# Kernel optimization log

Measured on AMD Instinct MI355X. Metric: run time of the kernel, lower is better.

The kernel has to match this reference:

```python
import jax, jax.numpy as jnp
import numpy as np

H, W = 800, 800          # map height/width (Encoder init args)
B, N, SD = 1, 100000, 32 # batch, entity_num, scatter_dim
C = 8                    # number of spatial grids
SPATIAL = (120, 120)     # SPATIAL_SIZE


def setup_inputs() -> dict:
    key = jax.random.key(0)
    ks = jax.random.split(key, 8)
    return {
        "spatial": jax.random.normal(ks[0], (C, H, W), jnp.float32) * 200.0,
        "project_embeddings": jax.random.normal(ks[1], (B, N, SD), jnp.float32),
        "locations": jax.random.randint(ks[2], (B, N, 2), 0, 800, jnp.int64 if jax.config.jax_enable_x64 else jnp.int32),
        "scalar": jax.random.normal(ks[3], (B, 8), jnp.float32),
        "w1": jax.random.normal(ks[4], (8, 32), jnp.float32) * 0.35,
        "b1": jnp.zeros((32,), jnp.float32),
        "w2": jax.random.normal(ks[5], (32, 4), jnp.float32) * 0.25,
        "b2": jnp.zeros((4,), jnp.float32),
    }


def _scatter_connection(project_embeddings, locations):
    # project_embeddings: [B, N, SD], locations: [B, N, 2] (x, y) ints
    loc = locations.reshape(-1, 2)
    x = jnp.clip(loc[:, 0], 0, W - 1)
    y = jnp.clip(loc[:, 1], 0, H - 1)
    bias = jnp.repeat(jnp.arange(B, dtype=x.dtype), N) * (H * W)
    idx = y * W + x + bias                       # [B*N] flat indices into B*H*W
    src = project_embeddings.reshape(-1, SD).T   # [SD, B*N]
    smap = jnp.zeros((SD, B * H * W), project_embeddings.dtype)
    smap = smap.at[:, idx].add(src)              # duplicate-safe scatter_add
    smap = smap.reshape(SD, B, H, W).transpose(1, 0, 2, 3)  # [B, SD, H, W]
    return jax.image.resize(smap, (B, SD) + SPATIAL, method="bilinear")


def _process_grids(spatial):
    # crop is the full map (grid of ones -> all rows/cols kept)
    arr = jnp.nan_to_num(spatial, posinf=0.0)
    arr = jnp.where(arr > 255.0, 255.0, arr) / 255.0
    arr = jnp.rot90(arr, k=1, axes=(1, 2))       # torch rot90 default: CCW in last-2 dims
    arr = jax.image.resize(arr, (C,) + SPATIAL, method="bilinear")
    return arr.astype(jnp.float32)[None]         # [1, C, 120, 120]


def reference(spatial, project_embeddings, locations, scalar, w1, b1, w2, b2):
    scatter_entity = _scatter_connection(project_embeddings, locations)  # [B,32,120,120]
    processed_spatial = _process_grids(spatial)                          # [1, C,120,120]
    final_spatial = jnp.concatenate([processed_spatial, scatter_entity], axis=1)
    scalar_embeddings = jax.nn.relu(scalar @ w1 + b1)
    scalar_embeddings = jax.nn.relu(scalar_embeddings @ w2 + b2)
    return final_spatial, scalar_embeddings
```

## Files before the change

### kernel.cpp

```cpp
#include <hip/hip_runtime.h>
#include <hip/hip_bf16.h>
#include <math.h>

#define HMAP 800
#define WMAP 800
#define OHW  120
#define NCELL (OHW * OHW)
#define NCH  8
#define NPTS 100000
#define SDIM 32
#define CAP  16
#define NBIN1 121
#define NBINS (NBIN1 * NBIN1)

__device__ __forceinline__ float rscale() { return 800.0f / 120.0f; }

__device__ __forceinline__ float clipval(float v) {
    if (isnan(v)) v = 0.f;
    else if (isinf(v)) v = (v > 0.f) ? 0.f : -3.4028234663852886e38f;
    if (v > 255.f) v = 255.f;
    return v;
}

__device__ __forceinline__ float norm_sum(int i) {
    const float r = rscale();
    float c = ((float)i + 0.5f) * r - 0.5f;
    int j0 = (int)ceilf(c - r);
    float s = 0.f;
#pragma unroll
    for (int k = 0; k < 14; ++k) {
        int j = j0 + k;
        if (j < 0 || j >= HMAP) continue;
        s += fmaxf(0.f, 1.f - fabsf(c - (float)j) / r);
    }
    return s;
}

#define WS_COUNTS   0
#define WS_SPILLCUR 14641
#define WS_INVS     14656
#define WS_ENTRIES  14784
#define WS_SPILL    (WS_ENTRIES + NBINS * CAP * 2)
#define WS_T        (WS_SPILL + NPTS * 2)
#define WS_END      (WS_T + NCH * WMAP * OHW)
#define WS_REQ_BYTES ((size_t)WS_END * 4)

#define Z_BLOCKS    58
#define FILLB       ((NPTS + 1023) / 1024)
#define RY_BLOCKS   (NCH * WMAP / 2)
#define GA_BLOCKS   (NCELL / 4)
#define RX_BLOCKS   (NCH * OHW / 2)

__global__ void k_zero(int* __restrict__ counts, float* __restrict__ invS) {
    int gid = blockIdx.x * 256 + threadIdx.x;
    if (gid < 14656) counts[gid] = 0;
    if (gid < OHW) invS[gid] = 1.0f / norm_sum(gid);
}

__global__ void k_phase1(const float* __restrict__ spatial, const int* __restrict__ loc,
                         float* __restrict__ T, int* __restrict__ counts,
                         int2* __restrict__ entries, int2* __restrict__ spill,
                         int* __restrict__ spill_cur) {
    __shared__ float row[2][HMAP];
    if (blockIdx.x < FILLB) {
        int base = blockIdx.x * 1024 + threadIdx.x;
        const float r = rscale();
#pragma unroll
        for (int k = 0; k < 4; ++k) {
            int n = base + k * 256;
            if (n >= NPTS) break;
            int2 xy = ((const int2*)loc)[n];
            int x = min(max(xy.x, 0), WMAP - 1);
            int y = min(max(xy.y, 0), HMAP - 1);
            int iy0 = (int)floorf(((float)y + 0.5f) / r - 0.5f);
            int ix0 = (int)floorf(((float)x + 0.5f) / r - 0.5f);
            int bin = (iy0 + 1) * NBIN1 + (ix0 + 1);
            int pos = (y << 10) | x;
            int slot = atomicAdd(&counts[bin], 1);
            if (slot < CAP) {
                entries[(size_t)bin * CAP + slot] = make_int2(n, pos);
            } else {
                int s = atomicAdd(spill_cur, 1);
                if (s < NPTS) spill[s] = make_int2((bin << 17) | n, pos);
            }
        }
        return;
    }
    int bx = (blockIdx.x - FILLB) * 2 + (threadIdx.x >> 7);
    int hw = threadIdx.x & 127;
    int rsel = threadIdx.x >> 7;
    int c = bx / WMAP, xx = bx % WMAP;
    const float* rp = spatial + (size_t)c * (HMAP * WMAP) + (size_t)xx * WMAP;
    for (int j = hw; j < HMAP; j += 128) row[rsel][j] = clipval(rp[j]);
    __syncthreads();
    int oy = hw;
    if (oy >= OHW) return;
    const float r = rscale();
    const float invR = 1.0f / r;
    float cy = ((float)oy + 0.5f) * r - 0.5f;
    int y0 = (int)ceilf(cy - r);
    float acc = 0.f, ws = 0.f;
#pragma unroll
    for (int k = 0; k < 14; ++k) {
        int j = y0 + k;
        float w = fmaxf(0.f, fmaf(-fabsf(cy - (float)j), invR, 1.f));
        w = (j >= 0 && j < HMAP) ? w : 0.f;
        int jc = min(max(j, 0), HMAP - 1);
        ws += w;
        acc = fmaf(w, row[rsel][HMAP - 1 - jc], acc);
    }
    T[((size_t)c * WMAP + xx) * OHW + oy] = acc / (255.f * ws);
}

__global__ void k_phase2(const float* __restrict__ T, const float* __restrict__ emb,
                         const int* __restrict__ counts, const int2* __restrict__ entries,
                         const int2* __restrict__ spill, const int* __restrict__ spill_cur,
                         const float* __restrict__ invS, float* __restrict__ out,
                         const float* __restrict__ scalar, const float* __restrict__ w1,
                         const float* __restrict__ b1, const float* __restrict__ w2,
                         const float* __restrict__ b2) {
    __shared__ int2 st[4][4][CAP];
    __shared__ float sh[32];
    int bid = blockIdx.x;
    if (bid < GA_BLOCKS) {
        int sbid = (bid & 7) * (GA_BLOCKS / 8) + (bid >> 3);
        int t = threadIdx.x;
        int wv = t >> 6;
        int cell = sbid * 4 + wv;
        int lane = t & 63;
        int g = lane >> 4;
        int c2 = lane & 15;
        int iy = cell / OHW, ix = cell % OHW;
        const float r = rscale();
        const float invR = 1.0f / r;
        float cy = ((float)iy + 0.5f) * r - 0.5f;
        float cx = ((float)ix + 0.5f) * r - 0.5f;
        float invS2 = invS[iy] * invS[ix];
        int b00 = iy * NBIN1 + ix;

        int mybin = b00 + (g >> 1) * NBIN1 + (g & 1);
        int craw = counts[mybin];
        bool ovfany = __any(craw > CAP);
        int cnt = min(craw, CAP);
        int cmax = cnt;
        cmax = max(cmax, __shfl_xor(cmax, 16));
        cmax = max(cmax, __shfl_xor(cmax, 32));

        {
            int gs = lane >> 4;
            int slot = lane & 15;
            int binst = b00 + (gs >> 1) * NBIN1 + (gs & 1);
            int2 e = entries[(size_t)(b00 + (lane >> 5) * NBIN1) * CAP + (lane & 31)];
            int scnt = min(counts[binst], CAP);
            int idx = 0;
            float w = 0.f;
            if (slot < scnt) {
                float py = (float)((e.y >> 10) & 1023);
                float px = (float)(e.y & 1023);
                float wy = fmaxf(0.f, fmaf(-fabsf(cy - py), invR, 1.f));
                float wx = fmaxf(0.f, fmaf(-fabsf(cx - px), invR, 1.f));
                w = wy * wx * invS2;
                idx = e.x;
            }
            st[wv][gs][slot] = make_int2(idx, __float_as_int(w));
        }

        const float2* embp = (const float2*)emb;
        float ax = 0.f, ay = 0.f;
        for (int i = 0; i < cmax; i += 4) {
            int2 s0 = st[wv][g][i + 0];
            int2 s1 = st[wv][g][i + 1];
            int2 s2 = st[wv][g][i + 2];
            int2 s3 = st[wv][g][i + 3];
            float2 v0 = embp[(size_t)s0.x * (SDIM / 2) + c2];
            float2 v1 = embp[(size_t)s1.x * (SDIM / 2) + c2];
            float2 v2 = embp[(size_t)s2.x * (SDIM / 2) + c2];
            float2 v3 = embp[(size_t)s3.x * (SDIM / 2) + c2];
            float w0 = __int_as_float(s0.y), w1_ = __int_as_float(s1.y);
            float w2_ = __int_as_float(s2.y), w3 = __int_as_float(s3.y);
            ax = fmaf(w0, v0.x, ax); ay = fmaf(w0, v0.y, ay);
            ax = fmaf(w1_, v1.x, ax); ay = fmaf(w1_, v1.y, ay);
            ax = fmaf(w2_, v2.x, ax); ay = fmaf(w2_, v2.y, ay);
            ax = fmaf(w3, v3.x, ax); ay = fmaf(w3, v3.y, ay);
        }

        if (ovfany) {
            int sn = min(spill_cur[0], NPTS);
            for (int s = 0; s < sn; ++s) {
                int2 e = spill[s];
                if ((e.x >> 17) == mybin) {
                    int n = e.x & 0x1FFFF;
                    float py = (float)((e.y >> 10) & 1023);
                    float px = (float)(e.y & 1023);
                    float wy = fmaxf(0.f, fmaf(-fabsf(cy - py), invR, 1.f));
                    float wx = fmaxf(0.f, fmaf(-fabsf(cx - px), invR, 1.f));
                    float w = wy * wx * invS2;
                    float2 v = embp[(size_t)n * (SDIM / 2) + c2];
                    ax = fmaf(w, v.x, ax); ay = fmaf(w, v.y, ay);
                }
            }
        }

        ax += __shfl_xor(ax, 16); ay += __shfl_xor(ay, 16);
        ax += __shfl_xor(ax, 32); ay += __shfl_xor(ay, 32);
        if (lane < 16) {
            out[(size_t)(NCH + 2 * c2) * NCELL + cell] = ax;
            out[(size_t)(NCH + 2 * c2 + 1) * NCELL + cell] = ay;
        }
        return;
    }
    if (bid < GA_BLOCKS + RX_BLOCKS) {
        int col = (bid - GA_BLOCKS) * 2 + (threadIdx.x >> 7);
        int oy = threadIdx.x & 127;
        if (oy >= OHW) return;
        int c = col / OHW, ox = col % OHW;
        const float r = rscale();
        const float invR = 1.0f / r;
        float cx = ((float)ox + 0.5f) * r - 0.5f;
        int x0 = (int)ceilf(cx - r);
        float acc = 0.f;
#pragma unroll
        for (int k = 0; k < 14; ++k) {
            int j = x0 + k;
            float w = fmaxf(0.f, fmaf(-fabsf(cx - (float)j), invR, 1.f));
            w = (j >= 0 && j < WMAP) ? w : 0.f;
            int jc = min(max(j, 0), WMAP - 1);
            acc = fmaf(w, T[((size_t)c * WMAP + jc) * OHW + oy], acc);
        }
        out[((size_t)c * OHW + oy) * OHW + ox] = acc * invS[ox];
        return;
    }
    int j = threadIdx.x;
    if (j < 32) {
        float a = b1[j];
        for (int i = 0; i < 8; ++i) a = fmaf(scalar[i], w1[i * 32 + j], a);
        sh[j] = fmaxf(a, 0.f);
    }
    __syncthreads();
    if (j < 4) {
        float a = b2[j];
        for (int i = 0; i < 32; ++i) a = fmaf(sh[i], w2[i * 4 + j], a);
        out[(size_t)(NCH + SDIM) * NCELL + j] = fmaxf(a, 0.f);
    }
}

__global__ void k_norm_fb(float* __restrict__ S) {
    int i = blockIdx.x * blockDim.x + threadIdx.x;
    if (i < OHW) S[i] = norm_sum(i);
}

__global__ void k_spatial_fb(const float* __restrict__ spatial, const float* __restrict__ S,
                             float* __restrict__ out) {
    int t = blockIdx.x * blockDim.x + threadIdx.x;
    if (t >= NCH * NCELL) return;
    int c = t / NCELL, rem = t % NCELL;
    int oy = rem / OHW, ox = rem % OHW;
    const float r = rscale();
    float cy = ((float)oy + 0.5f) * r - 0.5f;
    float cx = ((float)ox + 0.5f) * r - 0.5f;
    int y0 = (int)ceilf(cy - r);
    int x0 = (int)ceilf(cx - r);
    const float* sp = spatial + (size_t)c * (HMAP * WMAP);
    float acc = 0.f;
    for (int kx = 0; kx < 14; ++kx) {
        int col = x0 + kx;
        if (col < 0 || col >= WMAP) continue;
        float wxx = fmaxf(0.f, 1.f - fabsf(cx - (float)col) / r);
        if (wxx == 0.f) continue;
        const float* colp = sp + (size_t)col * WMAP;
        float accy = 0.f;
        for (int ky = 0; ky < 14; ++ky) {
            int j = y0 + ky;
            if (j < 0 || j >= HMAP) continue;
            float wyy = fmaxf(0.f, 1.f - fabsf(cy - (float)j) / r);
            accy = fmaf(wyy, clipval(colp[HMAP - 1 - j]), accy);
        }
        acc = fmaf(wxx, accy, acc);
    }
    out[t] = acc * (1.0f / 255.0f) / (S[oy] * S[ox]);
}

__global__ void k_scatter_fb(const float* __restrict__ emb, const int* __restrict__ loc,
                             const float* __restrict__ S, float* __restrict__ out) {
    int t = blockIdx.x * blockDim.x + threadIdx.x;
    if (t >= NPTS * SDIM) return;
    int n = t >> 5, c = t & 31;
    int x = min(max(loc[2 * n + 0], 0), WMAP - 1);
    int y = min(max(loc[2 * n + 1], 0), HMAP - 1);
    float e = emb[t];
    const float r = rscale();
    int iy0 = (int)floorf(((float)y + 0.5f) / r - 0.5f);
    int ix0 = (int)floorf(((float)x + 0.5f) / r - 0.5f);
    float* base = out + (size_t)(NCH + c) * NCELL;
#pragma unroll
    for (int a = 0; a < 2; ++a) {
        int iy = iy0 + a;
        if (iy < 0 || iy >= OHW) continue;
        float cyv = ((float)iy + 0.5f) * r - 0.5f;
        float wy = fmaxf(0.f, 1.f - fabsf(cyv - (float)y) / r) / S[iy];
#pragma unroll
        for (int b = 0; b < 2; ++b) {
            int ix = ix0 + b;
            if (ix < 0 || ix >= OHW) continue;
            float cxv = ((float)ix + 0.5f) * r - 0.5f;
            float wx = fmaxf(0.f, 1.f - fabsf(cxv - (float)x) / r) / S[ix];
            atomicAdd(base + iy * OHW + ix, e * wy * wx);
        }
    }
}

__global__ void k_mlp_fb(const float* __restrict__ scalar, const float* __restrict__ w1,
                         const float* __restrict__ b1, const float* __restrict__ w2,
                         const float* __restrict__ b2, float* __restrict__ out) {
    __shared__ float h[32];
    int j = threadIdx.x;
    if (j < 32) {
        float a = b1[j];
        for (int i = 0; i < 8; ++i) a = fmaf(scalar[i], w1[i * 32 + j], a);
        h[j] = fmaxf(a, 0.f);
    }
    __syncthreads();
    if (j < 4) {
        float a = b2[j];
        for (int i = 0; i < 32; ++i) a = fmaf(h[i], w2[i * 4 + j], a);
        out[(size_t)(NCH + SDIM) * NCELL + j] = fmaxf(a, 0.f);
    }
}

extern "C" void kernel_launch(void* const* d_in, const int* in_sizes, int n_in,
                              void* d_out, int out_size, void* d_ws, size_t ws_size,
                              hipStream_t stream) {
    const float* spatial = (const float*)d_in[0];
    const float* emb     = (const float*)d_in[1];
    const int*   loc     = (const int*)d_in[2];
    const float* scalar  = (const float*)d_in[3];
    const float* w1      = (const float*)d_in[4];
    const float* b1      = (const float*)d_in[5];
    const float* w2      = (const float*)d_in[6];
    const float* b2      = (const float*)d_in[7];
    float* out = (float*)d_out;

    int*   wsi = (int*)d_ws;
    float* wsf = (float*)d_ws;

    if (ws_size >= WS_REQ_BYTES) {
        int*   counts    = wsi + WS_COUNTS;
        int*   spill_cur = wsi + WS_SPILLCUR;
        float* invS      = wsf + WS_INVS;
        int2*  entries   = (int2*)(wsi + WS_ENTRIES);
        int2*  spill     = (int2*)(wsi + WS_SPILL);
        float* T         = wsf + WS_T;

        k_zero<<<Z_BLOCKS, 256, 0, stream>>>(counts, invS);
        k_phase1<<<FILLB + RY_BLOCKS, 256, 0, stream>>>(spatial, loc, T, counts,
                                                        entries, spill, spill_cur);
        k_phase2<<<GA_BLOCKS + RX_BLOCKS + 1, 256, 0, stream>>>(T, emb, counts, entries,
                                                                spill, spill_cur, invS,
                                                                out, scalar, w1, b1,
                                                                w2, b2);
    } else {
        float* S = wsf;
        hipMemsetAsync(d_out, 0, (size_t)out_size * sizeof(float), stream);
        k_norm_fb<<<1, 128, 0, stream>>>(S);
        k_spatial_fb<<<(NCH * NCELL + 255) / 256, 256, 0, stream>>>(spatial, S, out);
        k_scatter_fb<<<(NPTS * SDIM + 255) / 256, 256, 0, stream>>>(emb, loc, S, out);
        k_mlp_fb<<<1, 64, 0, stream>>>(scalar, w1, b1, w2, b2, out);
    }
}
```

Before: 33.89 us.

## Regroup kernel stages: separate fill, merge gather with y-resize, split x-resize

Reorganizes the three-kernel pipeline into four. The point-binning fill now runs alone. The entity gather is co-scheduled in one launch with the heavy y-direction resize of the spatial map, so the memory-bound resize can overlap with the atomic-light gather. The x-resize and MLP move to a final kernel. This adds a launch and makes the gather wait for the fill to finish, in exchange for better balancing of bandwidth-heavy and compute-heavy blocks.

```diff
diff --git a/kernel.cpp b/kernel.cpp
--- a/kernel.cpp
+++ b/kernel.cpp
@@ -57,70 +57,39 @@
     if (gid < OHW) invS[gid] = 1.0f / norm_sum(gid);
 }
 
-__global__ void k_phase1(const float* __restrict__ spatial, const int* __restrict__ loc,
-                         float* __restrict__ T, int* __restrict__ counts,
-                         int2* __restrict__ entries, int2* __restrict__ spill,
-                         int* __restrict__ spill_cur) {
+__global__ void k_fill(const int* __restrict__ loc, int* __restrict__ counts,
+                       int2* __restrict__ entries, int2* __restrict__ spill,
+                       int* __restrict__ spill_cur) {
+    int base = blockIdx.x * 1024 + threadIdx.x;
+    const float r = rscale();
+#pragma unroll
+    for (int k = 0; k < 4; ++k) {
+        int n = base + k * 256;
+        if (n >= NPTS) break;
+        int2 xy = ((const int2*)loc)[n];
+        int x = min(max(xy.x, 0), WMAP - 1);
+        int y = min(max(xy.y, 0), HMAP - 1);
+        int iy0 = (int)floorf(((float)y + 0.5f) / r - 0.5f);
+        int ix0 = (int)floorf(((float)x + 0.5f) / r - 0.5f);
+        int bin = (iy0 + 1) * NBIN1 + (ix0 + 1);
+        int pos = (y << 10) | x;
+        int slot = atomicAdd(&counts[bin], 1);
+        if (slot < CAP) {
+            entries[(size_t)bin * CAP + slot] = make_int2(n, pos);
+        } else {
+            int s = atomicAdd(spill_cur, 1);
+            if (s < NPTS) spill[s] = make_int2((bin << 17) | n, pos);
+        }
+    }
+}
+
+__global__ void k_gathery(const float* __restrict__ spatial, const float* __restrict__ emb,
+                          const int* __restrict__ counts, const int2* __restrict__ entries,
+                          const int2* __restrict__ spill, const int* __restrict__ spill_cur,
+                          const float* __restrict__ invS, float* __restrict__ T,
+                          float* __restrict__ out) {
+    __shared__ int2 st[4][4][CAP];
     __shared__ float row[2][HMAP];
-    if (blockIdx.x < FILLB) {
-        int base = blockIdx.x * 1024 + threadIdx.x;
-        const float r = rscale();
-#pragma unroll
-        for (int k = 0; k < 4; ++k) {
-            int n = base + k * 256;
-            if (n >= NPTS) break;
-            int2 xy = ((const int2*)loc)[n];
-            int x = min(max(xy.x, 0), WMAP - 1);
-            int y = min(max(xy.y, 0), HMAP - 1);
-            int iy0 = (int)floorf(((float)y + 0.5f) / r - 0.5f);
-            int ix0 = (int)floorf(((float)x + 0.5f) / r - 0.5f);
-            int bin = (iy0 + 1) * NBIN1 + (ix0 + 1);
-            int pos = (y << 10) | x;
-            int slot = atomicAdd(&counts[bin], 1);
-            if (slot < CAP) {
-                entries[(size_t)bin * CAP + slot] = make_int2(n, pos);
-            } else {
-                int s = atomicAdd(spill_cur, 1);
-                if (s < NPTS) spill[s] = make_int2((bin << 17) | n, pos);
-            }
-        }
-        return;
-    }
-    int bx = (blockIdx.x - FILLB) * 2 + (threadIdx.x >> 7);
-    int hw = threadIdx.x & 127;
-    int rsel = threadIdx.x >> 7;
-    int c = bx / WMAP, xx = bx % WMAP;
-    const float* rp = spatial + (size_t)c * (HMAP * WMAP) + (size_t)xx * WMAP;
-    for (int j = hw; j < HMAP; j += 128) row[rsel][j] = clipval(rp[j]);
-    __syncthreads();
-    int oy = hw;
-    if (oy >= OHW) return;
-    const float r = rscale();
-    const float invR = 1.0f / r;
-    float cy = ((float)oy + 0.5f) * r - 0.5f;
-    int y0 = (int)ceilf(cy - r);
-    float acc = 0.f, ws = 0.f;
-#pragma unroll
-    for (int k = 0; k < 14; ++k) {
-        int j = y0 + k;
-        float w = fmaxf(0.f, fmaf(-fabsf(cy - (float)j), invR, 1.f));
-        w = (j >= 0 && j < HMAP) ? w : 0.f;
-        int jc = min(max(j, 0), HMAP - 1);
-        ws += w;
-        acc = fmaf(w, row[rsel][HMAP - 1 - jc], acc);
-    }
-    T[((size_t)c * WMAP + xx) * OHW + oy] = acc / (255.f * ws);
-}
-
-__global__ void k_phase2(const float* __restrict__ T, const float* __restrict__ emb,
-                         const int* __restrict__ counts, const int2* __restrict__ entries,
-                         const int2* __restrict__ spill, const int* __restrict__ spill_cur,
-                         const float* __restrict__ invS, float* __restrict__ out,
-                         const float* __restrict__ scalar, const float* __restrict__ w1,
-                         const float* __restrict__ b1, const float* __restrict__ w2,
-                         const float* __restrict__ b2) {
-    __shared__ int2 st[4][4][CAP];
-    __shared__ float sh[32];
     int bid = blockIdx.x;
     if (bid < GA_BLOCKS) {
         int sbid = (bid & 7) * (GA_BLOCKS / 8) + (bid >> 3);
@@ -209,8 +178,41 @@
         }
         return;
     }
-    if (bid < GA_BLOCKS + RX_BLOCKS) {
-        int col = (bid - GA_BLOCKS) * 2 + (threadIdx.x >> 7);
+    int bx = (bid - GA_BLOCKS) * 2 + (threadIdx.x >> 7);
+    int hw = threadIdx.x & 127;
+    int rsel = threadIdx.x >> 7;
+    int c = bx / WMAP, xx = bx % WMAP;
+    const float* rp = spatial + (size_t)c * (HMAP * WMAP) + (size_t)xx * WMAP;
+    for (int j = hw; j < HMAP; j += 128) row[rsel][j] = clipval(rp[j]);
+    __syncthreads();
+    int oy = hw;
+    if (oy >= OHW) return;
+    const float r = rscale();
+    const float invR = 1.0f / r;
+    float cy = ((float)oy + 0.5f) * r - 0.5f;
+    int y0 = (int)ceilf(cy - r);
+    float acc = 0.f, ws = 0.f;
+#pragma unroll
+    for (int k = 0; k < 14; ++k) {
+        int j = y0 + k;
+        float w = fmaxf(0.f, fmaf(-fabsf(cy - (float)j), invR, 1.f));
+        w = (j >= 0 && j < HMAP) ? w : 0.f;
+        int jc = min(max(j, 0), HMAP - 1);
+        ws += w;
+        acc = fmaf(w, row[rsel][HMAP - 1 - jc], acc);
+    }
+    T[((size_t)c * WMAP + xx) * OHW + oy] = acc / (255.f * ws);
+}
+
+__global__ void k_rx(const float* __restrict__ T, const float* __restrict__ invS,
+                     float* __restrict__ out,
+                     const float* __restrict__ scalar, const float* __restrict__ w1,
+                     const float* __restrict__ b1, const float* __restrict__ w2,
+                     const float* __restrict__ b2) {
+    __shared__ float sh[32];
+    int bid = blockIdx.x;
+    if (bid < RX_BLOCKS) {
+        int col = bid * 2 + (threadIdx.x >> 7);
         int oy = threadIdx.x & 127;
         if (oy >= OHW) return;
         int c = col / OHW, ox = col % OHW;
@@ -352,12 +354,11 @@
         float* T         = wsf + WS_T;
 
         k_zero<<<Z_BLOCKS, 256, 0, stream>>>(counts, invS);
-        k_phase1<<<FILLB + RY_BLOCKS, 256, 0, stream>>>(spatial, loc, T, counts,
-                                                        entries, spill, spill_cur);
-        k_phase2<<<GA_BLOCKS + RX_BLOCKS + 1, 256, 0, stream>>>(T, emb, counts, entries,
-                                                                spill, spill_cur, invS,
-                                                                out, scalar, w1, b1,
-                                                                w2, b2);
+        k_fill<<<FILLB, 256, 0, stream>>>(loc, counts, entries, spill, spill_cur);
+        k_gathery<<<GA_BLOCKS + RY_BLOCKS, 256, 0, stream>>>(spatial, emb, counts,
+                                                             entries, spill, spill_cur,
+                                                             invS, T, out);
+        k_rx<<<RX_BLOCKS + 1, 256, 0, stream>>>(T, invS, out, scalar, w1, b1, w2, b2);
     } else {
         float* S = wsf;
         hipMemsetAsync(d_out, 0, (size_t)out_size * sizeof(float), stream);
```

Measured after the change: 41.16 us. 1.21x slower.
